# Performance work log

Measured on AMD Instinct MI355X. Metric: run time of the kernel, lower is better.

## Reference

```python
import jax, jax.numpy as jnp
import numpy as np

CHANNELS = [32, 64, 96, 128]   # out_channels_list (slimmable widths)
G = len(CHANNELS)              # channel_gate_num
C = CHANNELS[-1]
TAU = 1.0
EPS = 1e-5
# MASK[i, c] = 1 if c < CHANNELS[i]; gate @ MASK reproduces the per-width
# accumulation loop in apply_differentiable_gate_channel exactly.
MASK = jnp.asarray(np.arange(C)[None, :] < np.asarray(CHANNELS)[:, None], dtype=np.float32)


def _gate_apply(x, gate):
    # apply_differentiable_gate_channel: NaN-mask then gated channel slicing
    x = jnp.where(jnp.isnan(x), jnp.zeros_like(x), x)
    mult = gate @ MASK                      # [B, C]
    return x * mult[:, :, None]


def setup_inputs() -> dict:
    key = jax.random.key(0)
    ks = jax.random.split(key, 9)
    B, L = 16, 32768
    x = jax.random.normal(ks[0], (B, C, L), jnp.float32)
    gumbel_noise = jax.random.gumbel(ks[1], (B, G), jnp.float32)
    w_gate = jax.random.normal(ks[2], (G, C), jnp.float32) * 0.05          # 1x1 gate conv
    conv_w = jax.random.normal(ks[3], (C, C), jnp.float32) / np.sqrt(C)    # DSpwConv1d weight [out,in]
    conv_b = jax.random.normal(ks[4], (C,), jnp.float32) * 0.01
    bn_w = 1.0 + 0.1 * jax.random.normal(ks[5], (C,), jnp.float32)
    bn_b = 0.01 * jax.random.normal(ks[6], (C,), jnp.float32)
    # per-width running stats, zero-padded beyond each width (as in DSBatchNorm1d)
    rmean = 0.1 * jax.random.normal(ks[7], (G, C), jnp.float32) * MASK
    rvar = jax.random.uniform(ks[8], (G, C), jnp.float32, 0.5, 1.5) * MASK
    return dict(x=x, gumbel_noise=gumbel_noise, w_gate=w_gate, conv_w=conv_w,
                conv_b=conv_b, bn_w=bn_w, bn_b=bn_b, rmean=rmean, rvar=rvar)


def reference(x, gumbel_noise, w_gate, conv_w, conv_b, bn_w, bn_b, rmean, rvar):
    B = x.shape[0]
    # --- MultiHeadGate: global average pool over length, 1x1 conv -> logits ---
    pool = jnp.mean(x, axis=-1)                          # [B, C]
    logits = pool @ w_gate.T                             # [B, G]
    # --- gumbel_softmax (straight-through hard gate) ---
    y = (logits + gumbel_noise) / TAU
    y_soft = jax.nn.softmax(y, axis=1)
    idx = jnp.argmax(y_soft, axis=1)
    y_hard = jax.nn.one_hot(idx, G, dtype=y_soft.dtype)
    gate = y_hard - jax.lax.stop_gradient(y_soft) + y_soft  # [B, G]
    # --- DSpwConv1d dynamic mode: full-width pointwise conv, then channel gating ---
    out = jnp.einsum('bil,oi->bol', x, conv_w) + conv_b[None, :, None]
    out = _gate_apply(out, gate)
    # --- DSBatchNorm1d dynamic mode: matmul-combined per-width running stats ---
    mean = gate @ rmean                                  # [B, C]
    var = gate @ rvar                                    # [B, C]
    xn = (out - mean[:, :, None]) / jnp.sqrt(var[:, :, None] + EPS)
    xn = xn * bn_w[None, :, None] + bn_b[None, :, None]
    return _gate_apply(xn, gate)
```

## Files before the change

kernel.cpp:

```cpp
#include <hip/hip_runtime.h>

#define CC   128
#define GG   4
#define BB   16
#define LL   32768
#define TL   128
#define EPSV 1e-5f
#define WROW 136

typedef short short8 __attribute__((ext_vector_type(8)));
typedef float f32x16 __attribute__((ext_vector_type(16)));

__device__ inline unsigned short f2bf(float f) {
    union { float f; unsigned int u; } v; v.f = f;
    unsigned int r = (v.u + 0x7FFF + ((v.u >> 16) & 1)) >> 16;
    return (unsigned short)r;
}

__global__ __launch_bounds__(256) void pool_kernel(const float* __restrict__ x,
                                                   float* __restrict__ pool) {
    const int row = blockIdx.x;
    const float4* xr = (const float4*)(x + (size_t)row * LL);
    const int t = threadIdx.x;
    float s = 0.f;
#pragma unroll
    for (int k = 0; k < (LL / 4) / 256; ++k) {
        float4 v = xr[t + k * 256];
        s += (v.x + v.y) + (v.z + v.w);
    }
    for (int off = 32; off > 0; off >>= 1) s += __shfl_down(s, off, 64);
    __shared__ float red[4];
    if ((t & 63) == 0) red[t >> 6] = s;
    __syncthreads();
    if (t == 0) pool[row] = (red[0] + red[1] + red[2] + red[3]) * (1.0f / LL);
}

__global__ __launch_bounds__(256) void gate_kernel(const float* __restrict__ pool,
                                                   const float* __restrict__ gumbel,
                                                   const float* __restrict__ w_gate,
                                                   const float* __restrict__ conv_b,
                                                   const float* __restrict__ bn_w,
                                                   const float* __restrict__ bn_b,
                                                   const float* __restrict__ rmean,
                                                   const float* __restrict__ rvar,
                                                   float* __restrict__ Acoef,
                                                   float* __restrict__ Tcoef) {
    __shared__ float yl[BB][GG];
    __shared__ int   sidx[BB];
    const int t = threadIdx.x;
    if (t < BB * GG) {
        const int b = t / GG, g = t % GG;
        float s = 0.f;
        for (int c = 0; c < CC; ++c) s += pool[b * CC + c] * w_gate[g * CC + c];
        yl[b][g] = s + gumbel[b * GG + g];
    }
    __syncthreads();
    if (t < BB) {
        int best = 0; float bv = yl[t][0];
        for (int g = 1; g < GG; ++g) { if (yl[t][g] > bv) { bv = yl[t][g]; best = g; } }
        sidx[t] = best;
    }
    __syncthreads();
    for (int i = t; i < BB * CC; i += 256) {
        const int b = i / CC, c = i % CC;
        const int g = sidx[b];
        const int width = 32 * (g + 1);
        float a = 0.f, tt = 0.f;
        if (c < width) {
            const float inv = rsqrtf(rvar[g * CC + c] + EPSV);
            const float s = bn_w[c] * inv;
            a = s;
            tt = (conv_b[c] - rmean[g * CC + c]) * s + bn_b[c];
        }
        Acoef[i] = a;
        Tcoef[i] = tt;
    }
}

__global__ __launch_bounds__(256, 4) void conv_kernel(const float* __restrict__ x,
                                                      const float* __restrict__ conv_w,
                                                      const float* __restrict__ Acoef,
                                                      const float* __restrict__ Tcoef,
                                                      float* __restrict__ out) {
    __shared__ unsigned short xlds[TL * WROW];
    __shared__ float sA[CC], sT[CC];

    const int b  = blockIdx.y;
    const int l0 = blockIdx.x * TL;
    const int t  = threadIdx.x;
    const int lane = t & 63;
    const int og   = t >> 6;
    const int m  = lane & 31;
    const int kh = lane >> 5;

    if (t < CC) { sA[t] = Acoef[b * CC + t]; sT[t] = Tcoef[b * CC + t]; }

    short8 wfrag[8];
    {
        const float* wr = conv_w + (og * 32 + m) * CC + kh * 8;
#pragma unroll
        for (int ks = 0; ks < 8; ++ks) {
            const float4 a = *(const float4*)(wr + ks * 16);
            const float4 c = *(const float4*)(wr + ks * 16 + 4);
            short8 f;
            f[0] = (short)f2bf(a.x); f[1] = (short)f2bf(a.y);
            f[2] = (short)f2bf(a.z); f[3] = (short)f2bf(a.w);
            f[4] = (short)f2bf(c.x); f[5] = (short)f2bf(c.y);
            f[6] = (short)f2bf(c.z); f[7] = (short)f2bf(c.w);
            wfrag[ks] = f;
        }
    }

    const float* xb = x + (size_t)b * CC * LL + l0;
#pragma unroll
    for (int it = 0; it < 16; ++it) {
        const int idx = it * 256 + t;
        const int l  = idx & 127;
        const int i0 = (idx >> 7) * 4;
        const float v0 = xb[(size_t)(i0 + 0) * LL + l];
        const float v1 = xb[(size_t)(i0 + 1) * LL + l];
        const float v2 = xb[(size_t)(i0 + 2) * LL + l];
        const float v3 = xb[(size_t)(i0 + 3) * LL + l];
        ushort4 u;
        u.x = f2bf(v0); u.y = f2bf(v1); u.z = f2bf(v2); u.w = f2bf(v3);
        *(ushort4*)&xlds[l * WROW + i0] = u;
    }
    __syncthreads();

    f32x16 acc[4];
#pragma unroll
    for (int nt = 0; nt < 4; ++nt)
#pragma unroll
        for (int r = 0; r < 16; ++r) acc[nt][r] = 0.f;

#pragma unroll
    for (int ks = 0; ks < 8; ++ks) {
#pragma unroll
        for (int nt = 0; nt < 4; ++nt) {
            const short8 bf = *(const short8*)&xlds[(nt * 32 + m) * WROW + ks * 16 + kh * 8];
            acc[nt] = __builtin_amdgcn_mfma_f32_32x32x16_bf16(wfrag[ks], bf, acc[nt], 0, 0, 0);
        }
    }

    float sreg[16], treg[16];
#pragma unroll
    for (int r = 0; r < 16; ++r) {
        const int o = og * 32 + (r & 3) + 8 * (r >> 2) + 4 * kh;
        sreg[r] = sA[o]; treg[r] = sT[o];
    }
    float* ob = out + (size_t)b * CC * LL + l0;
#pragma unroll
    for (int nt = 0; nt < 4; ++nt) {
#pragma unroll
        for (int r = 0; r < 16; ++r) {
            const int o = og * 32 + (r & 3) + 8 * (r >> 2) + 4 * kh;
            __builtin_nontemporal_store(fmaf(acc[nt][r], sreg[r], treg[r]),
                                        ob + (size_t)o * LL + nt * 32 + m);
        }
    }
}

extern "C" void kernel_launch(void* const* d_in, const int* in_sizes, int n_in,
                              void* d_out, int out_size, void* d_ws, size_t ws_size,
                              hipStream_t stream) {
    const float* x      = (const float*)d_in[0];
    const float* gumbel = (const float*)d_in[1];
    const float* w_gate = (const float*)d_in[2];
    const float* conv_w = (const float*)d_in[3];
    const float* conv_b = (const float*)d_in[4];
    const float* bn_w   = (const float*)d_in[5];
    const float* bn_b   = (const float*)d_in[6];
    const float* rmean  = (const float*)d_in[7];
    const float* rvar   = (const float*)d_in[8];
    float* out = (float*)d_out;

    float* pool  = (float*)d_ws;
    float* Acoef = pool + BB * CC;
    float* Tcoef = Acoef + BB * CC;

    pool_kernel<<<BB * CC, 256, 0, stream>>>(x, pool);
    gate_kernel<<<1, 256, 0, stream>>>(pool, gumbel, w_gate, conv_b, bn_w, bn_b,
                                       rmean, rvar, Acoef, Tcoef);
    conv_kernel<<<dim3(LL / TL, BB), 256, 0, stream>>>(x, conv_w, Acoef, Tcoef, out);
}
```

Before: 129.0 us.

## Fuse pooling with bf16 transpose pre-pass and feed conv via global-to-LDS loads

Measured after the change: 302.3 us. 2.34x slower.

```diff
diff --git a/kernel.cpp b/kernel.cpp
--- a/kernel.cpp
+++ b/kernel.cpp
@@ -5,8 +5,8 @@
 #define BB   16
 #define LL   32768
 #define TL   128
+#define NTL  256
 #define EPSV 1e-5f
-#define WROW 136
 
 typedef short short8 __attribute__((ext_vector_type(8)));
 typedef float f32x16 __attribute__((ext_vector_type(16)));
@@ -17,22 +17,57 @@
     return (unsigned short)r;
 }
 
-__global__ __launch_bounds__(256) void pool_kernel(const float* __restrict__ x,
-                                                   float* __restrict__ pool) {
-    const int row = blockIdx.x;
-    const float4* xr = (const float4*)(x + (size_t)row * LL);
-    const int t = threadIdx.x;
-    float s = 0.f;
-#pragma unroll
-    for (int k = 0; k < (LL / 4) / 256; ++k) {
-        float4 v = xr[t + k * 256];
-        s += (v.x + v.y) + (v.z + v.w);
-    }
-    for (int off = 32; off > 0; off >>= 1) s += __shfl_down(s, off, 64);
-    __shared__ float red[4];
-    if ((t & 63) == 0) red[t >> 6] = s;
-    __syncthreads();
-    if (t == 0) pool[row] = (red[0] + red[1] + red[2] + red[3]) * (1.0f / LL);
+__device__ inline void gl_lds16(const void* g, void* l) {
+    __builtin_amdgcn_global_load_lds(
+        (const __attribute__((address_space(1))) unsigned int*)g,
+        (__attribute__((address_space(3))) unsigned int*)l, 16, 0, 0);
+}
+
+__global__ __launch_bounds__(256) void prep_kernel(const float* __restrict__ x,
+                                                   float* __restrict__ pool,
+                                                   unsigned short* __restrict__ xT) {
+    __shared__ float tile[64 * 128];
+    const int ltile = blockIdx.x;
+    const int cbase = blockIdx.y * 64;
+    const int b     = blockIdx.z;
+    const int t  = threadIdx.x;
+    const int l0 = ltile * TL;
+    const float* xb = x + (size_t)b * CC * LL;
+
+#pragma unroll
+    for (int it = 0; it < 8; ++it) {
+        const int idx = it * 256 + t;
+        const int lc  = idx >> 5;
+        const int q   = (idx & 31) * 4;
+        const float4 v = *(const float4*)(xb + (size_t)(cbase + lc) * LL + l0 + q);
+        float s = (v.x + v.y) + (v.z + v.w);
+        s += __shfl_down(s, 16, 32);
+        s += __shfl_down(s, 8, 32);
+        s += __shfl_down(s, 4, 32);
+        s += __shfl_down(s, 2, 32);
+        s += __shfl_down(s, 1, 32);
+        if ((t & 31) == 0) atomicAdd(&pool[b * CC + cbase + lc], s);
+        const int swzA = ((lc >> 2) & 7) << 2;
+        *(float4*)&tile[lc * 128 + (q ^ swzA)] = v;
+    }
+    __syncthreads();
+
+    char* xTt = (char*)xT + (size_t)(b * NTL + ltile) * (TL * CC * 2);
+#pragma unroll
+    for (int it = 0; it < 8; ++it) {
+        const int idx = it * 256 + t;
+        const int l  = idx >> 4;
+        const int co = (idx & 15) * 4;
+        const int swzA = ((co >> 2) & 7) << 2;
+        const float v0 = tile[(co + 0) * 128 + (l ^ swzA)];
+        const float v1 = tile[(co + 1) * 128 + (l ^ swzA)];
+        const float v2 = tile[(co + 2) * 128 + (l ^ swzA)];
+        const float v3 = tile[(co + 3) * 128 + (l ^ swzA)];
+        ushort4 u;
+        u.x = f2bf(v0); u.y = f2bf(v1); u.z = f2bf(v2); u.w = f2bf(v3);
+        const int boff = ((cbase + co) * 2) ^ ((l & 7) << 4);
+        *(ushort4*)(xTt + (size_t)l * 256 + boff) = u;
+    }
 }
 
 __global__ __launch_bounds__(256) void gate_kernel(const float* __restrict__ pool,
@@ -52,7 +87,7 @@
         const int b = t / GG, g = t % GG;
         float s = 0.f;
         for (int c = 0; c < CC; ++c) s += pool[b * CC + c] * w_gate[g * CC + c];
-        yl[b][g] = s + gumbel[b * GG + g];
+        yl[b][g] = s * (1.0f / LL) + gumbel[b * GG + g];
     }
     __syncthreads();
     if (t < BB) {
@@ -77,21 +112,26 @@
     }
 }
 
-__global__ __launch_bounds__(256, 4) void conv_kernel(const float* __restrict__ x,
+__global__ __launch_bounds__(256, 4) void conv_kernel(const unsigned short* __restrict__ xT,
                                                       const float* __restrict__ conv_w,
                                                       const float* __restrict__ Acoef,
                                                       const float* __restrict__ Tcoef,
                                                       float* __restrict__ out) {
-    __shared__ unsigned short xlds[TL * WROW];
+    __shared__ unsigned short xlds[TL * CC];
     __shared__ float sA[CC], sT[CC];
 
-    const int b  = blockIdx.y;
-    const int l0 = blockIdx.x * TL;
+    const int tile = (NTL - 1) - blockIdx.x;
+    const int b    = (BB - 1) - blockIdx.y;
     const int t  = threadIdx.x;
     const int lane = t & 63;
     const int og   = t >> 6;
     const int m  = lane & 31;
     const int kh = lane >> 5;
+
+    const char* src = (const char*)xT + (size_t)(b * NTL + tile) * (TL * CC * 2);
+#pragma unroll
+    for (int it = 0; it < 8; ++it)
+        gl_lds16(src + it * 4096 + t * 16, (char*)xlds + it * 4096 + t * 16);
 
     if (t < CC) { sA[t] = Acoef[b * CC + t]; sT[t] = Tcoef[b * CC + t]; }
 
@@ -110,21 +150,6 @@
             wfrag[ks] = f;
         }
     }
-
-    const float* xb = x + (size_t)b * CC * LL + l0;
-#pragma unroll
-    for (int it = 0; it < 16; ++it) {
-        const int idx = it * 256 + t;
-        const int l  = idx & 127;
-        const int i0 = (idx >> 7) * 4;
-        const float v0 = xb[(size_t)(i0 + 0) * LL + l];
-        const float v1 = xb[(size_t)(i0 + 1) * LL + l];
-        const float v2 = xb[(size_t)(i0 + 2) * LL + l];
-        const float v3 = xb[(size_t)(i0 + 3) * LL + l];
-        ushort4 u;
-        u.x = f2bf(v0); u.y = f2bf(v1); u.z = f2bf(v2); u.w = f2bf(v3);
-        *(ushort4*)&xlds[l * WROW + i0] = u;
-    }
     __syncthreads();
 
     f32x16 acc[4];
@@ -137,7 +162,9 @@
     for (int ks = 0; ks < 8; ++ks) {
 #pragma unroll
         for (int nt = 0; nt < 4; ++nt) {
-            const short8 bf = *(const short8*)&xlds[(nt * 32 + m) * WROW + ks * 16 + kh * 8];
+            const int row  = nt * 32 + m;
+            const int koff = (ks * 32 + kh * 16) ^ ((row & 7) << 4);
+            const short8 bf = *(const short8*)((const char*)xlds + row * 256 + koff);
             acc[nt] = __builtin_amdgcn_mfma_f32_32x32x16_bf16(wfrag[ks], bf, acc[nt], 0, 0, 0);
         }
     }
@@ -148,7 +175,7 @@
         const int o = og * 32 + (r & 3) + 8 * (r >> 2) + 4 * kh;
         sreg[r] = sA[o]; treg[r] = sT[o];
     }
-    float* ob = out + (size_t)b * CC * LL + l0;
+    float* ob = out + (size_t)b * CC * LL + tile * TL;
 #pragma unroll
     for (int nt = 0; nt < 4; ++nt) {
 #pragma unroll
@@ -177,9 +204,11 @@
     float* pool  = (float*)d_ws;
     float* Acoef = pool + BB * CC;
     float* Tcoef = Acoef + BB * CC;
-
-    pool_kernel<<<BB * CC, 256, 0, stream>>>(x, pool);
+    unsigned short* xT = (unsigned short*)((char*)d_ws + 65536);
+
+    hipMemsetAsync(pool, 0, BB * CC * sizeof(float), stream);
+    prep_kernel<<<dim3(NTL, 2, BB), 256, 0, stream>>>(x, pool, xT);
     gate_kernel<<<1, 256, 0, stream>>>(pool, gumbel, w_gate, conv_b, bn_w, bn_b,
                                        rmean, rvar, Acoef, Tcoef);
-    conv_kernel<<<dim3(LL / TL, BB), 256, 0, stream>>>(x, conv_w, Acoef, Tcoef, out);
-}
+    conv_kernel<<<dim3(NTL, BB), 256, 0, stream>>>(xT, conv_w, Acoef, Tcoef, out);
+}
```
